# Kernel tuning notes

Measured on AMD Instinct MI355X. Metric: run time of the kernel, lower is better.

Reference implementation:

```python
import jax, jax.numpy as jnp
import numpy as np

N_NODES = 50000
N_EDGES = 800000
F_IN = 64
F_HID = 64
K = 3


def _cheb_norm(edge_index, edge_weight, n):
    # PyG ChebConv sym normalization with lambda_max=2: Lhat = -D^{-1/2} A D^{-1/2}
    # (diagonal of Lhat is exactly 0, so self-loop terms vanish)
    row, col = edge_index[0], edge_index[1]
    deg = jax.ops.segment_sum(edge_weight, row, num_segments=n)
    dis = jnp.where(deg > 0, jax.lax.rsqrt(jnp.where(deg > 0, deg, 1.0)), 0.0)
    return -dis[row] * edge_weight * dis[col]


def _prop(x, row, col, norm, n):
    # out[i] = sum_{e: col[e]=i} norm[e] * x[row[e]]
    return jax.ops.segment_sum(x[row] * norm[:, None], col, num_segments=n)


def _cheb_conv(x, W, b, row, col, norm, n):
    # ChebConv K=3: Tx0=x, Tx1=Lhat x, Tx2=2 Lhat Tx1 - Tx0
    tx0 = x
    tx1 = _prop(x, row, col, norm, n)
    tx2 = 2.0 * _prop(tx1, row, col, norm, n) - tx0
    return tx0 @ W[0] + tx1 @ W[1] + tx2 @ W[2] + b


def setup_inputs() -> dict:
    key = jax.random.key(0)
    ks = jax.random.split(key, 20)
    inp = {
        "x": jax.random.normal(ks[0], (N_NODES, F_IN), dtype=jnp.float32),
        "edge_index": jax.random.randint(ks[1], (2, N_EDGES), 0, N_NODES, dtype=jnp.int32),
        "edge_weight": jax.random.uniform(ks[2], (N_EDGES,), dtype=jnp.float32),
    }
    # 6 ChebConvs: x->gate (F_IN->F_HID) and h->gate (F_HID->F_HID) for z, r, h
    names_in = [("Wxz", "bxz", F_IN), ("Whz", "bhz", F_HID), ("Wxr", "bxr", F_IN),
                ("Whr", "bhr", F_HID), ("Wxh", "bxh", F_IN), ("Whh", "bhh", F_HID)]
    for i, (wn, bn, fin) in enumerate(names_in):
        scale = 1.0 / np.sqrt(fin)
        inp[wn] = jax.random.normal(ks[3 + i], (K, fin, F_HID), dtype=jnp.float32) * scale
        inp[bn] = jnp.zeros((F_HID,), dtype=jnp.float32)
    inp["Wlin"] = jax.random.normal(ks[12], (F_HID, 2), dtype=jnp.float32) * (1.0 / np.sqrt(F_HID))
    inp["blin"] = jnp.zeros((2,), dtype=jnp.float32)
    return inp


def reference(x, edge_index, edge_weight, Wxz, bxz, Whz, bhz, Wxr, bxr, Whr, bhr,
              Wxh, bxh, Whh, bhh, Wlin, blin):
    n = x.shape[0]
    row, col = edge_index[0], edge_index[1]
    norm = _cheb_norm(edge_index, edge_weight, n)
    h0 = jnp.zeros((n, F_HID), dtype=x.dtype)
    # GConvGRU single step (initial hidden state = 0)
    z = jax.nn.sigmoid(_cheb_conv(x, Wxz, bxz, row, col, norm, n)
                       + _cheb_conv(h0, Whz, bhz, row, col, norm, n))
    r = jax.nn.sigmoid(_cheb_conv(x, Wxr, bxr, row, col, norm, n)
                       + _cheb_conv(h0, Whr, bhr, row, col, norm, n))
    h_tilde = jnp.tanh(_cheb_conv(x, Wxh, bxh, row, col, norm, n)
                       + _cheb_conv(h0 * r, Whh, bhh, row, col, norm, n))
    h = z * h0 + (1.0 - z) * h_tilde
    # head: dropout in eval mode (identity) -> tanh -> linear -> sigmoid
    return jax.nn.sigmoid(jnp.tanh(h) @ Wlin + blin)
```

## Files before the change

kernel.cpp:

```cpp
#include <hip/hip_runtime.h>
#include <hip/hip_bf16.h>

#define N_NODES 50000
#define N_EDGES 800000
#define NB1 400
#define CH  2000
#define NBKT 196
#define CAP 8192
#define SORT_MAX 6144

typedef unsigned short ushort_t;
typedef unsigned long long u64;
typedef __attribute__((ext_vector_type(8))) short bf16x8;
typedef __attribute__((ext_vector_type(4))) float f32x4;

constexpr int GCUR_O  = 0;
constexpr int DIS_O   = 512;
constexpr int OFF_O   = 50512;
constexpr int CSLOT_O = 100544;
constexpr int RSLOT_O = 3311808;
constexpr int RW_O    = 4917440;
constexpr int ABUF_O  = 6517440;
constexpr int PBUF_O  = 11317440;
constexpr int XS_O    = 11329728;
constexpr int T1S_O   = RSLOT_O;

__device__ __forceinline__ ushort_t f32_to_bf16(float f) {
    unsigned u = __float_as_uint(f);
    u += 0x7fffu + ((u >> 16) & 1u);
    return (ushort_t)(u >> 16);
}
__device__ __forceinline__ float bflo(unsigned u) { return __uint_as_float(u << 16); }
__device__ __forceinline__ float bfhi(unsigned u) { return __uint_as_float(u & 0xffff0000u); }
__device__ __forceinline__ unsigned packbf2(float a, float b) {
    return (unsigned)f32_to_bf16(a) | ((unsigned)f32_to_bf16(b) << 16);
}
__device__ __forceinline__ float fsigmoid(float x) { return 1.f / (1.f + __expf(-x)); }
__device__ __forceinline__ float ftanh(float x) {
    x = fminf(15.f, fmaxf(-15.f, x));
    float e = __expf(2.f * x);
    return (e - 1.f) / (e + 1.f);
}

__device__ __forceinline__ unsigned block_scan256_incl(unsigned v, int t, unsigned* wsum) {
    int lane = t & 63;
    unsigned sc = v;
#pragma unroll
    for (int o = 1; o < 64; o <<= 1) {
        unsigned u = __shfl_up(sc, o, 64);
        if (lane >= o) sc += u;
    }
    if (t < 256 && lane == 63) wsum[t >> 6] = sc;
    __syncthreads();
    if (t < 256) {
        int wid = t >> 6;
        unsigned off = 0;
#pragma unroll
        for (int wv = 0; wv < 3; ++wv) if (wv < wid) off += wsum[wv];
        sc += off;
    }
    __syncthreads();
    return sc;
}

__global__ __launch_bounds__(512) void k1(
    const int* __restrict__ ei, const float* __restrict__ ew,
    const float* __restrict__ Wxz, const float* __restrict__ Wxh,
    unsigned* __restrict__ gcur, u64* __restrict__ cslot,
    unsigned* __restrict__ rslot, ushort_t* __restrict__ pbuf) {
    int bid = blockIdx.x, t = threadIdx.x;
    if (bid < NB1) {
        __shared__ unsigned colbuf[CH], rowbuf[CH];
        __shared__ unsigned hc[256], hr[256], bc[256], br[256];
        if (t < 256) { hc[t] = 0; hr[t] = 0; }
        __syncthreads();
        int e0 = bid * CH;
        for (int i = t; i < CH; i += 512) {
            unsigned r = (unsigned)ei[e0 + i];
            unsigned c = (unsigned)ei[N_EDGES + e0 + i];
            rowbuf[i] = r;
            colbuf[i] = c;
            atomicAdd(&hc[c >> 8], 1u);
            atomicAdd(&hr[r >> 8], 1u);
        }
        __syncthreads();
        if (t < NBKT) {
            bc[t] = atomicAdd(&gcur[t], hc[t]);
            br[t] = atomicAdd(&gcur[256 + t], hr[t]);
        }
        __syncthreads();
        if (t < 256) { hc[t] = 0; hr[t] = 0; }
        __syncthreads();
        for (int i = t; i < CH; i += 512) {
            unsigned c = colbuf[i];
            unsigned r = rowbuf[i];
            unsigned w = __float_as_uint(ew[e0 + i]);
            unsigned dc = c >> 8;
            unsigned pc = bc[dc] + atomicAdd(&hc[dc], 1u);
            if (pc < CAP)
                cslot[(size_t)dc * CAP + pc] = ((u64)w << 32) | ((c & 255u) << 16) | (r & 0xFFFFu);
            unsigned dr = r >> 8;
            unsigned pr = br[dr] + atomicAdd(&hr[dr], 1u);
            if (pr < CAP) rslot[(size_t)dr * CAP + pr] = (w & 0xFFFFFF00u) | (r & 255u);
        }
    } else {
        for (int idx = t; idx < 24576; idx += 512) {
            int k = idx >> 7, n = idx & 127;
            float v = (n < 64) ? Wxz[k * 64 + n] : Wxh[k * 64 + (n - 64)];
            int c = n >> 4, s = k >> 5, l = (((k >> 3) & 3) << 4) | (n & 15), j = k & 7;
            pbuf[((c * 6 + s) * 64 + l) * 8 + j] = f32_to_bf16(v);
        }
    }
}

__global__ __launch_bounds__(512) void k2(
    const float* __restrict__ x, const unsigned* __restrict__ gcur,
    const u64* __restrict__ cslot, const unsigned* __restrict__ rslot,
    float* __restrict__ dis, int* __restrict__ off, u64* __restrict__ rw,
    unsigned* __restrict__ abuf, unsigned* __restrict__ xs) {
    int bid = blockIdx.x, t = threadIdx.x;
    __shared__ unsigned rawA[SORT_MAX], rawB[SORT_MAX];
    __shared__ unsigned hist[256], hsc[256], cur[256], gs[256];
    __shared__ unsigned wsum[8];
    __shared__ float facc[256];

    if (bid < NBKT) {
        unsigned szv = (t < NBKT) ? gcur[t] : 0u;
        unsigned inc = block_scan256_incl(szv, t, wsum);
        if (t < 256) gs[t] = inc - szv;
        if (t < 256) hist[t] = 0;
        __syncthreads();
        unsigned szb = gcur[bid];
        unsigned sz = min(szb, (unsigned)SORT_MAX);
        unsigned base = gs[bid];
        for (unsigned i = t; i < sz; i += 512) {
            u64 v = cslot[(size_t)bid * CAP + i];
            unsigned lo = (unsigned)v;
            rawA[i] = lo;
            rawB[i] = (unsigned)(v >> 32);
            atomicAdd(&hist[(lo >> 16) & 255u], 1u);
        }
        __syncthreads();
        unsigned h0 = (t < 256) ? hist[t] : 0u;
        unsigned hinc = block_scan256_incl(h0, t, wsum);
        if (t < 256) {
            hsc[t] = hinc - h0;
            cur[t] = 0u;
            int c = bid * 256 + t;
            if (c <= N_NODES) off[c] = (int)(base + hsc[t]);
        }
        __syncthreads();
        for (unsigned i = t; i < sz; i += 512) {
            unsigned lo = rawA[i];
            unsigned d = (lo >> 16) & 255u;
            unsigned p = hsc[d] + atomicAdd(&cur[d], 1u);
            rw[base + p] = ((u64)rawB[i] << 32) | (lo & 0xFFFFu);
        }
    } else {
        int b = bid - NBKT;
        if (t < 256) facc[t] = 0.f;
        __syncthreads();
        unsigned szr = min(gcur[256 + b], (unsigned)CAP);
        const unsigned* rs = rslot + (size_t)b * CAP;
        for (unsigned i = t; i < szr; i += 512)
            atomicAdd(&facc[rs[i] & 255u], __uint_as_float(rs[i] & 0xFFFFFF00u));
        __syncthreads();
        if (t < 256) {
            float d = facc[t];
            float r = d > 0.f ? rsqrtf(d) : 0.f;
            facc[t] = r;
            int n = b * 256 + t;
            if (n < N_NODES) dis[n] = r;
        }
        __syncthreads();
        for (int idx = t; idx < 8192; idx += 512) {
            int nl = idx >> 5, q = idx & 31;
            int n = b * 256 + nl;
            if (n < N_NODES) {
                float2 xv = ((const float2*)x)[n * 32 + q];
                float r = facc[nl];
                abuf[n * 96 + q] = packbf2(xv.x, xv.y);
                xs[n * 32 + q] = packbf2(r * xv.x, r * xv.y);
            }
        }
    }
}

__global__ __launch_bounds__(256) void k_prop(
    const int* __restrict__ off, const u64* __restrict__ rw,
    const unsigned* __restrict__ xsrc, const float* __restrict__ dis,
    const float* __restrict__ xf, unsigned* __restrict__ abuf,
    unsigned* __restrict__ t1s, int mode) {
    int node = (blockIdx.x * 256 + threadIdx.x) >> 6;
    if (node >= N_NODES) return;
    int lane = threadIdx.x & 63, h = lane >> 5, q = lane & 31;
    int b = off[node], end = off[node + 1];
    float di = dis[node];
    float acc0 = 0.f, acc1 = 0.f;
    for (; b + 7 < end; b += 8) {
        u64 v0 = rw[b + h], v1 = rw[b + h + 2], v2 = rw[b + h + 4], v3 = rw[b + h + 6];
        unsigned u0 = xsrc[((unsigned)v0 & 0xFFFFu) * 32 + q];
        unsigned u1 = xsrc[((unsigned)v1 & 0xFFFFu) * 32 + q];
        unsigned u2 = xsrc[((unsigned)v2 & 0xFFFFu) * 32 + q];
        unsigned u3 = xsrc[((unsigned)v3 & 0xFFFFu) * 32 + q];
        float a0 = __uint_as_float((unsigned)(v0 >> 32));
        float a1 = __uint_as_float((unsigned)(v1 >> 32));
        float a2 = __uint_as_float((unsigned)(v2 >> 32));
        float a3 = __uint_as_float((unsigned)(v3 >> 32));
        acc0 += a0 * bflo(u0) + a1 * bflo(u1) + a2 * bflo(u2) + a3 * bflo(u3);
        acc1 += a0 * bfhi(u0) + a1 * bfhi(u1) + a2 * bfhi(u2) + a3 * bfhi(u3);
    }
    for (; b + 1 < end; b += 2) {
        u64 v = rw[b + h];
        unsigned u = xsrc[((unsigned)v & 0xFFFFu) * 32 + q];
        float a = __uint_as_float((unsigned)(v >> 32));
        acc0 += a * bflo(u); acc1 += a * bfhi(u);
    }
    if (b < end && h == 0) {
        u64 v = rw[b];
        unsigned u = xsrc[((unsigned)v & 0xFFFFu) * 32 + q];
        float a = __uint_as_float((unsigned)(v >> 32));
        acc0 += a * bflo(u); acc1 += a * bfhi(u);
    }
    acc0 += __shfl_xor(acc0, 32, 64);
    acc1 += __shfl_xor(acc1, 32, 64);
    if (h == 0) {
        float t0 = -di * acc0, t1v = -di * acc1;
        if (mode == 0) {
            abuf[node * 96 + 32 + q] = packbf2(t0, t1v);
            t1s[node * 32 + q] = packbf2(di * t0, di * t1v);
        } else {
            float2 xv = ((const float2*)xf)[node * 32 + q];
            abuf[node * 96 + 64 + q] = packbf2(2.f * t0 - xv.x, 2.f * t1v - xv.y);
        }
    }
}

__global__ __launch_bounds__(256) void k_gemm(
    const ushort_t* __restrict__ ab, const ushort_t* __restrict__ pbuf,
    const float* __restrict__ bxz, const float* __restrict__ bhz,
    const float* __restrict__ bxh, const float* __restrict__ bhh,
    const float* __restrict__ Wlin, const float* __restrict__ blin,
    float2* __restrict__ out) {
    __shared__ ushort_t bsh[24576];
    int tid = threadIdx.x;
    {
        uint4* s4 = (uint4*)bsh;
        const uint4* g4 = (const uint4*)pbuf;
        for (int i = tid; i < 3072; i += 256) s4[i] = g4[i];
    }
    __syncthreads();

    int wave = tid >> 6, lane = tid & 63;
    int quad = lane >> 4, m = lane & 15;

    float bzv[4], bhv[4], wl0[4], wl1[4];
#pragma unroll
    for (int c = 0; c < 4; ++c) {
        int col = c * 16 + m;
        bzv[c] = bxz[col] + bhz[col];
        bhv[c] = bxh[col] + bhh[col];
        wl0[c] = Wlin[2 * col];
        wl1[c] = Wlin[2 * col + 1];
    }
    float bl0 = blin[0], bl1 = blin[1];

    for (int tile = 0; tile < 2; ++tile) {
        int n0 = (blockIdx.x * 2 + tile) * 64;
        int arow = n0 + wave * 16 + m;
        const ushort_t* ap = ab + (size_t)arow * 192 + quad * 8;

        f32x4 acc[8];
#pragma unroll
        for (int c = 0; c < 8; ++c) acc[c] = (f32x4){0.f, 0.f, 0.f, 0.f};
#pragma unroll
        for (int s = 0; s < 6; ++s) {
            bf16x8 af = *(const bf16x8*)(ap + s * 32);
#pragma unroll
            for (int c = 0; c < 8; ++c) {
                bf16x8 bfr = *(const bf16x8*)(bsh + ((c * 6 + s) * 64 + lane) * 8);
                acc[c] = __builtin_amdgcn_mfma_f32_16x16x32_bf16(af, bfr, acc[c], 0, 0, 0);
            }
        }
#pragma unroll
        for (int i = 0; i < 4; ++i) {
            float p0 = 0.f, p1 = 0.f;
#pragma unroll
            for (int c = 0; c < 4; ++c) {
                float z  = fsigmoid(acc[c][i] + bzv[c]);
                float ht = ftanh(acc[c + 4][i] + bhv[c]);
                float t  = ftanh((1.f - z) * ht);
                p0 += t * wl0[c];
                p1 += t * wl1[c];
            }
            for (int o = 1; o <= 8; o <<= 1) {
                p0 += __shfl_xor(p0, o, 64);
                p1 += __shfl_xor(p1, o, 64);
            }
            int g = n0 + wave * 16 + quad * 4 + i;
            if (m == 0 && g < N_NODES)
                out[g] = make_float2(fsigmoid(p0 + bl0), fsigmoid(p1 + bl1));
        }
    }
}

extern "C" void kernel_launch(void* const* d_in, const int* in_sizes, int n_in,
                              void* d_out, int out_size, void* d_ws, size_t ws_size,
                              hipStream_t stream) {
    const float* x    = (const float*)d_in[0];
    const int*   ei   = (const int*)d_in[1];
    const float* ew   = (const float*)d_in[2];
    const float* Wxz  = (const float*)d_in[3];
    const float* bxz  = (const float*)d_in[4];
    const float* bhz  = (const float*)d_in[6];
    const float* Wxh  = (const float*)d_in[11];
    const float* bxh  = (const float*)d_in[12];
    const float* bhh  = (const float*)d_in[14];
    const float* Wlin = (const float*)d_in[15];
    const float* blin = (const float*)d_in[16];

    float*    ws    = (float*)d_ws;
    unsigned* gcur  = (unsigned*)(ws + GCUR_O);
    float*    dis   = ws + DIS_O;
    int*      off   = (int*)(ws + OFF_O);
    u64*      cslot = (u64*)(ws + CSLOT_O);
    unsigned* rslot = (unsigned*)(ws + RSLOT_O);
    u64*      rw    = (u64*)(ws + RW_O);
    unsigned* abuf  = (unsigned*)(ws + ABUF_O);
    ushort_t* pbuf  = (ushort_t*)(ws + PBUF_O);
    unsigned* xs    = (unsigned*)(ws + XS_O);
    unsigned* t1s   = (unsigned*)(ws + T1S_O);

    hipMemsetAsync(d_ws, 0, 512 * 4, stream);

    k1<<<NB1 + 1, 512, 0, stream>>>(ei, ew, Wxz, Wxh, gcur, cslot, rslot, pbuf);
    k2<<<NBKT * 2, 512, 0, stream>>>(x, gcur, cslot, rslot, dis, off, rw, abuf, xs);
    k_prop<<<12500, 256, 0, stream>>>(off, rw, xs, dis, x, abuf, t1s, 0);
    k_prop<<<12500, 256, 0, stream>>>(off, rw, t1s, dis, x, abuf, abuf, 1);
    k_gemm<<<391, 256, 0, stream>>>((const ushort_t*)abuf, pbuf, bxz, bhz, bxh, bhh,
                                    Wlin, blin, (float2*)d_out);
}
```

Measured before the change: 216.3 us.

## Locally sort edges by bucket in LDS before coalesced scatter to global

In the bucketing kernel, each block now counting-sorts its edge chunk by column and row bucket in shared memory. It then writes each bucket's edges as contiguous runs into cslot/rslot, replacing the previous per-edge random global scatter. In the sort kernel, the second pass stages sorted entries in LDS and writes rw sequentially instead of scattering directly to global. This trades extra LDS passes, more barriers and more shared memory for better-coalesced global writes. The added shared memory may reduce occupancy.

```diff
diff --git a/kernel.cpp b/kernel.cpp
--- a/kernel.cpp
+++ b/kernel.cpp
@@ -69,18 +69,22 @@
     unsigned* __restrict__ gcur, u64* __restrict__ cslot,
     unsigned* __restrict__ rslot, ushort_t* __restrict__ pbuf) {
     int bid = blockIdx.x, t = threadIdx.x;
+    __shared__ u64 pC[CH];
+    __shared__ ushort_t ordC[CH], ordR[CH];
+    __shared__ unsigned char digC[CH], digR[CH];
+    __shared__ unsigned hc[256], hr[256], scC[256], scR[256], bc[256], br[256];
+    __shared__ unsigned wsum[8];
     if (bid < NB1) {
-        __shared__ unsigned colbuf[CH], rowbuf[CH];
-        __shared__ unsigned hc[256], hr[256], bc[256], br[256];
         if (t < 256) { hc[t] = 0; hr[t] = 0; }
         __syncthreads();
         int e0 = bid * CH;
         for (int i = t; i < CH; i += 512) {
             unsigned r = (unsigned)ei[e0 + i];
             unsigned c = (unsigned)ei[N_EDGES + e0 + i];
-            rowbuf[i] = r;
-            colbuf[i] = c;
-            atomicAdd(&hc[c >> 8], 1u);
+            unsigned w = __float_as_uint(ew[e0 + i]);
+            unsigned dc = c >> 8;
+            pC[i] = ((u64)w << 32) | (dc << 24) | ((c & 255u) << 16) | (r & 0xFFFFu);
+            atomicAdd(&hc[dc], 1u);
             atomicAdd(&hr[r >> 8], 1u);
         }
         __syncthreads();
@@ -88,20 +92,40 @@
             bc[t] = atomicAdd(&gcur[t], hc[t]);
             br[t] = atomicAdd(&gcur[256 + t], hr[t]);
         }
-        __syncthreads();
-        if (t < 256) { hc[t] = 0; hr[t] = 0; }
+        unsigned vC = (t < 256) ? hc[t] : 0u;
+        unsigned vR = (t < 256) ? hr[t] : 0u;
+        unsigned iC = block_scan256_incl(vC, t, wsum);
+        unsigned iR = block_scan256_incl(vR, t, wsum);
+        if (t < 256) {
+            scC[t] = iC - vC;
+            scR[t] = iR - vR;
+            hc[t] = 0; hr[t] = 0;
+        }
         __syncthreads();
         for (int i = t; i < CH; i += 512) {
-            unsigned c = colbuf[i];
-            unsigned r = rowbuf[i];
-            unsigned w = __float_as_uint(ew[e0 + i]);
-            unsigned dc = c >> 8;
-            unsigned pc = bc[dc] + atomicAdd(&hc[dc], 1u);
-            if (pc < CAP)
-                cslot[(size_t)dc * CAP + pc] = ((u64)w << 32) | ((c & 255u) << 16) | (r & 0xFFFFu);
+            u64 p = pC[i];
+            unsigned dc = (unsigned)(p >> 24) & 255u;
+            unsigned pc = scC[dc] + atomicAdd(&hc[dc], 1u);
+            ordC[pc] = (ushort_t)i;
+            digC[pc] = (unsigned char)dc;
+            unsigned r = (unsigned)p & 0xFFFFu;
             unsigned dr = r >> 8;
-            unsigned pr = br[dr] + atomicAdd(&hr[dr], 1u);
-            if (pr < CAP) rslot[(size_t)dr * CAP + pr] = (w & 0xFFFFFF00u) | (r & 255u);
+            unsigned pr = scR[dr] + atomicAdd(&hr[dr], 1u);
+            ordR[pr] = (ushort_t)i;
+            digR[pr] = (unsigned char)dr;
+        }
+        __syncthreads();
+        for (int i = t; i < CH; i += 512) {
+            unsigned dc = digC[i];
+            u64 p = pC[ordC[i]];
+            unsigned slotC = bc[dc] + (unsigned)i - scC[dc];
+            if (slotC < CAP) cslot[(size_t)dc * CAP + slotC] = p;
+            unsigned dr = digR[i];
+            u64 q = pC[ordR[i]];
+            unsigned slotR = br[dr] + (unsigned)i - scR[dr];
+            if (slotR < CAP)
+                rslot[(size_t)dr * CAP + slotR] =
+                    ((unsigned)(q >> 32) & 0xFFFFFF00u) | ((unsigned)q & 255u);
         }
     } else {
         for (int idx = t; idx < 24576; idx += 512) {
@@ -119,7 +143,7 @@
     float* __restrict__ dis, int* __restrict__ off, u64* __restrict__ rw,
     unsigned* __restrict__ abuf, unsigned* __restrict__ xs) {
     int bid = blockIdx.x, t = threadIdx.x;
-    __shared__ unsigned rawA[SORT_MAX], rawB[SORT_MAX];
+    __shared__ u64 srt[SORT_MAX];
     __shared__ unsigned hist[256], hsc[256], cur[256], gs[256];
     __shared__ unsigned wsum[8];
     __shared__ float facc[256];
@@ -133,13 +157,9 @@
         unsigned szb = gcur[bid];
         unsigned sz = min(szb, (unsigned)SORT_MAX);
         unsigned base = gs[bid];
-        for (unsigned i = t; i < sz; i += 512) {
-            u64 v = cslot[(size_t)bid * CAP + i];
-            unsigned lo = (unsigned)v;
-            rawA[i] = lo;
-            rawB[i] = (unsigned)(v >> 32);
-            atomicAdd(&hist[(lo >> 16) & 255u], 1u);
-        }
+        const u64* cs = cslot + (size_t)bid * CAP;
+        for (unsigned i = t; i < sz; i += 512)
+            atomicAdd(&hist[((unsigned)cs[i] >> 16) & 255u], 1u);
         __syncthreads();
         unsigned h0 = (t < 256) ? hist[t] : 0u;
         unsigned hinc = block_scan256_incl(h0, t, wsum);
@@ -151,10 +171,15 @@
         }
         __syncthreads();
         for (unsigned i = t; i < sz; i += 512) {
-            unsigned lo = rawA[i];
-            unsigned d = (lo >> 16) & 255u;
+            u64 v = cs[i];
+            unsigned d = ((unsigned)v >> 16) & 255u;
             unsigned p = hsc[d] + atomicAdd(&cur[d], 1u);
-            rw[base + p] = ((u64)rawB[i] << 32) | (lo & 0xFFFFu);
+            srt[p] = v;
+        }
+        __syncthreads();
+        for (unsigned i = t; i < sz; i += 512) {
+            u64 v = srt[i];
+            rw[base + i] = ((v >> 32) << 32) | ((unsigned)v & 0xFFFFu);
         }
     } else {
         int b = bid - NBKT;
```

After: 209.1 us. 3.3% less time.
